# Performance work log

Hardware: AMD Instinct MI355X
Metric: run time of the kernel (lower is better)

## Reference

```python
import jax, jax.numpy as jnp
import numpy as np

N_NODES = 50000
N_EDGES = 800000
IN_FEATS = 256
OUT_FEATS = 64
NUM_HEADS = 4
NEG_SLOPE = 0.2


def setup_inputs() -> dict:
    key = jax.random.key(0)
    k1, k2, k3, k4, k5, k6 = jax.random.split(key, 6)
    feat = jax.random.normal(k1, (N_NODES, IN_FEATS), dtype=jnp.float32)
    src = jax.random.randint(k2, (N_EDGES,), 0, N_NODES, dtype=jnp.int32)
    dst = jax.random.randint(k3, (N_EDGES,), 0, N_NODES, dtype=jnp.int32)
    # fc weight (no bias), xavier-like scale
    W = jax.random.normal(k4, (IN_FEATS, NUM_HEADS * OUT_FEATS), dtype=jnp.float32) * 0.05
    attn_l = jax.random.normal(k5, (NUM_HEADS, OUT_FEATS), dtype=jnp.float32) * 0.1
    attn_r = jax.random.normal(k6, (NUM_HEADS, OUT_FEATS), dtype=jnp.float32) * 0.1
    return {"feat": feat, "src": src, "dst": dst, "W": W, "attn_l": attn_l, "attn_r": attn_r}


def reference(feat, src, dst, W, attn_l, attn_r):
    N = feat.shape[0]
    # fc: [N, H*F] -> [N, H, F]
    ft = (feat @ W).reshape(N, NUM_HEADS, OUT_FEATS)
    # per-node attention logits [N, H]
    el = jnp.einsum('nhf,hf->nh', ft, attn_l)
    er = jnp.einsum('nhf,hf->nh', ft, attn_r)
    # edge logits: u_add_v then leaky relu  [E, H]
    e = el[src] + er[dst]
    e = jnp.where(e > 0, e, NEG_SLOPE * e)
    # edge softmax over edges sharing the same dst, numerically stable
    m = jax.ops.segment_max(e, dst, num_segments=N)          # [N, H]
    e_exp = jnp.exp(e - m[dst])                               # [E, H]
    denom = jax.ops.segment_sum(e_exp, dst, num_segments=N)  # [N, H]
    a = e_exp / denom[dst]                                    # [E, H]
    # u_mul_e + sum: gather src features, weight, scatter-add to dst
    msg = ft[src] * a[:, :, None]                             # [E, H, F]
    out = jax.ops.segment_sum(msg, dst, num_segments=N)      # [N, H, F]
    return out
```

## Files before the change

kernel.cpp:

```cpp
#include <hip/hip_runtime.h>
#include <hip/hip_bf16.h>
#include <math.h>

#define N_NODES 50000
#define N_EDGES 800000
#define IN_F 256
#define HF 256
#define NHEAD 4
#define OF 64
#define NPAD 50176
#define CAP 96
#define MPAD 50048
#define GEMM_BLOCKS 782
#define FILL_BLOCKS 1250
#define TOT_BLOCKS (GEMM_BLOCKS + FILL_BLOCKS)

typedef __attribute__((ext_vector_type(8))) short short8;
typedef __attribute__((ext_vector_type(4))) float f32x4;

__device__ __forceinline__ ushort f32_to_bf16(float x) {
  unsigned u = __float_as_uint(x);
  u += 0x7FFFu + ((u >> 16) & 1u);
  return (ushort)(u >> 16);
}
__device__ __forceinline__ float bfl(unsigned u) { return __uint_as_float(u << 16); }
__device__ __forceinline__ float bfh(unsigned u) { return __uint_as_float(u & 0xFFFF0000u); }

__global__ __launch_bounds__(256) void prep(const float* __restrict__ W,
                                            ushort* __restrict__ WT,
                                            int* __restrict__ cnt) {
  int i = blockIdx.x * blockDim.x + threadIdx.x;
  int stride = gridDim.x * blockDim.x;
  for (int j = i; j < IN_F * HF; j += stride) {
    int n = j >> 8, k = j & 255;
    WT[j] = f32_to_bf16(W[k * HF + n]);
  }
  for (int j = i; j < NPAD; j += stride) cnt[j] = 0;
}

__global__ __launch_bounds__(256) void fused_gf(const float* __restrict__ A,
                                                const ushort* __restrict__ BT,
                                                const float* __restrict__ al,
                                                const float* __restrict__ ar,
                                                ushort* __restrict__ C,
                                                float* __restrict__ el,
                                                float* __restrict__ er,
                                                const int* __restrict__ src,
                                                const int* __restrict__ dst,
                                                int* __restrict__ cnt,
                                                int* __restrict__ csr_src) {
  int tid = threadIdx.x;
  int i = blockIdx.x;
  int g0 = (int)(((long)i * GEMM_BLOCKS) / TOT_BLOCKS);
  int g1 = (int)(((long)(i + 1) * GEMM_BLOCKS) / TOT_BLOCKS);

  if (g1 == g0) {
    int fb = i - g0;
    int stride = FILL_BLOCKS * 256;
    for (int e = fb * 256 + tid; e < N_EDGES; e += stride) {
      int s = __builtin_nontemporal_load(&src[e]);
      int d = dst[e];
      int p = atomicAdd(&cnt[d], 1);
      if (p < CAP) csr_src[d * CAP + p] = s;
    }
    return;
  }

  int w = tid >> 6, lane = tid & 63;
  int brow = g0 * 64;
  int rl = lane & 15, khalf = lane >> 4;
  f32x4 acc[4][4];
#pragma unroll
  for (int m = 0; m < 4; ++m)
#pragma unroll
    for (int n = 0; n < 4; ++n) acc[m][n] = (f32x4){0.f, 0.f, 0.f, 0.f};

  int row[4];
#pragma unroll
  for (int m = 0; m < 4; ++m) row[m] = min(brow + m * 16 + rl, N_NODES - 1);

#pragma unroll 2
  for (int kt = 0; kt < 8; ++kt) {
    int k0 = kt * 32 + khalf * 8;
    short8 a[4], b[4];
#pragma unroll
    for (int m = 0; m < 4; ++m) {
      const float* ap = A + (size_t)row[m] * IN_F + k0;
      float4 lo = *(const float4*)(ap);
      float4 hi = *(const float4*)(ap + 4);
      union { short8 s; unsigned u[4]; } cv;
      cv.u[0] = __builtin_amdgcn_perm(__float_as_uint(lo.y), __float_as_uint(lo.x), 0x07060302);
      cv.u[1] = __builtin_amdgcn_perm(__float_as_uint(lo.w), __float_as_uint(lo.z), 0x07060302);
      cv.u[2] = __builtin_amdgcn_perm(__float_as_uint(hi.y), __float_as_uint(hi.x), 0x07060302);
      cv.u[3] = __builtin_amdgcn_perm(__float_as_uint(hi.w), __float_as_uint(hi.z), 0x07060302);
      a[m] = cv.s;
    }
#pragma unroll
    for (int n = 0; n < 4; ++n) {
      int c = w * 64 + n * 16 + rl;
      b[n] = *(const short8*)(BT + (size_t)c * IN_F + k0);
    }
#pragma unroll
    for (int m = 0; m < 4; ++m)
#pragma unroll
      for (int n = 0; n < 4; ++n)
        acc[m][n] = __builtin_amdgcn_mfma_f32_16x16x32_bf16(a[m], b[n], acc[m][n], 0, 0, 0);
  }

#pragma unroll
  for (int m = 0; m < 4; ++m) {
    int r0 = brow + m * 16 + khalf * 4;
#pragma unroll
    for (int n = 0; n < 4; ++n) {
      int col = w * 64 + n * 16 + rl;
#pragma unroll
      for (int j = 0; j < 4; ++j)
        if (r0 + j < N_NODES)
          C[(size_t)(r0 + j) * HF + col] = f32_to_bf16(acc[m][n][j]);
    }
  }

  float alv[4], arv[4];
#pragma unroll
  for (int n = 0; n < 4; ++n) {
    alv[n] = al[w * OF + n * 16 + rl];
    arv[n] = ar[w * OF + n * 16 + rl];
  }
#pragma unroll
  for (int m = 0; m < 4; ++m) {
    int r0 = brow + m * 16 + khalf * 4;
#pragma unroll
    for (int j = 0; j < 4; ++j) {
      float pl = acc[m][0][j] * alv[0] + acc[m][1][j] * alv[1] +
                 acc[m][2][j] * alv[2] + acc[m][3][j] * alv[3];
      float pr = acc[m][0][j] * arv[0] + acc[m][1][j] * arv[1] +
                 acc[m][2][j] * arv[2] + acc[m][3][j] * arv[3];
#pragma unroll
      for (int off2 = 1; off2 < 16; off2 <<= 1) {
        pl += __shfl_xor(pl, off2);
        pr += __shfl_xor(pr, off2);
      }
      int r = r0 + j;
      if (rl == 0 && r < N_NODES) {
        el[r * NHEAD + w] = pl;
        er[r * NHEAD + w] = pr;
      }
    }
  }
}

__global__ __launch_bounds__(256) void aggregate(const int* __restrict__ cnt,
                                                 const int* __restrict__ csr_src,
                                                 const float* __restrict__ el,
                                                 const float* __restrict__ er,
                                                 const ushort* __restrict__ ft,
                                                 float* __restrict__ out) {
  int w = threadIdx.x >> 6, lane = threadIdx.x & 63;
  int n = blockIdx.x * 4 + w;
  if (n >= N_NODES) return;
  int half = lane >> 5, l5 = lane & 31;
  int h = l5 >> 3;
  int c = l5 << 3;
  float erh = er[n * NHEAD + h];
  int j0 = n * CAP;
  int j1 = j0 + min(cnt[n], CAP);
  float a0 = 0.f, a1 = 0.f, a2 = 0.f, a3 = 0.f;
  float a4 = 0.f, a5 = 0.f, a6 = 0.f, a7 = 0.f;
  float den = 0.f;
#pragma unroll 4
  for (int j = j0 + half; j < j1; j += 2) {
    int s = __builtin_nontemporal_load(&csr_src[j]);
    float x = el[s * NHEAD + h] + erh;
    x = x > 0.f ? x : 0.2f * x;
    float a = __expf(x);
    den += a;
    uint4 u = *(const uint4*)(ft + (size_t)s * HF + c);
    a0 += bfl(u.x) * a; a1 += bfh(u.x) * a;
    a2 += bfl(u.y) * a; a3 += bfh(u.y) * a;
    a4 += bfl(u.z) * a; a5 += bfh(u.z) * a;
    a6 += bfl(u.w) * a; a7 += bfh(u.w) * a;
  }
  den += __shfl_xor(den, 32);
  a0 += __shfl_xor(a0, 32); a1 += __shfl_xor(a1, 32);
  a2 += __shfl_xor(a2, 32); a3 += __shfl_xor(a3, 32);
  a4 += __shfl_xor(a4, 32); a5 += __shfl_xor(a5, 32);
  a6 += __shfl_xor(a6, 32); a7 += __shfl_xor(a7, 32);
  if (half == 0) {
    float inv = den > 0.f ? 1.0f / den : 0.f;
    f32x4 r0 = {a0 * inv, a1 * inv, a2 * inv, a3 * inv};
    f32x4 r1 = {a4 * inv, a5 * inv, a6 * inv, a7 * inv};
    __builtin_nontemporal_store(r0, (f32x4*)&out[(size_t)n * HF + c]);
    __builtin_nontemporal_store(r1, (f32x4*)&out[(size_t)n * HF + c + 4]);
  }
}

extern "C" void kernel_launch(void* const* d_in, const int* in_sizes, int n_in,
                              void* d_out, int out_size, void* d_ws, size_t ws_size,
                              hipStream_t stream) {
  const float* feat = (const float*)d_in[0];
  const int*   src  = (const int*)d_in[1];
  const int*   dst  = (const int*)d_in[2];
  const float* W    = (const float*)d_in[3];
  const float* al   = (const float*)d_in[4];
  const float* ar   = (const float*)d_in[5];
  float* out = (float*)d_out;

  char* ws = (char*)d_ws;
  ushort* ft_bf   = (ushort*)(ws);
  int*    csr_src = (int*)(ws + 26000000);
  int*    cnt     = (int*)(ws + 45400000);
  float*  el      = (float*)(ws + 45700000);
  float*  er      = (float*)(ws + 46500000);
  ushort* WT      = (ushort*)(ws + 47300000);

  prep<<<512, 256, 0, stream>>>(W, WT, cnt);
  fused_gf<<<TOT_BLOCKS, 256, 0, stream>>>(feat, WT, al, ar, ft_bf,
                                           el, er, src, dst, cnt, csr_src);
  aggregate<<<(N_NODES + 3) / 4, 256, 0, stream>>>(cnt, csr_src, el, er, ft_bf, out);
}
```

Measured before the change: 151.9 us.

## Aggregate raw features before projection and fold attention vectors into W

Uses linearity to reorder the work. el/er are computed directly from the input features through precomputed W·attn vectors (a small 16-column MFMA), and the input is only converted to bf16. The aggregate kernel sums the raw 256-dim features per head with the softmax weights, stages the per-head sums in LDS, and then applies W with MFMA per 16-node tile. This removes the full N×256×256 GEMM ahead of aggregation and the separate ft buffer, but it quadruples the per-edge accumulation work (four heads times eight features per lane) and adds a GEMM on the aggregated results.

```diff
diff --git a/kernel.cpp b/kernel.cpp
--- a/kernel.cpp
+++ b/kernel.cpp
@@ -10,10 +10,9 @@
 #define OF 64
 #define NPAD 50176
 #define CAP 96
-#define MPAD 50048
-#define GEMM_BLOCKS 782
+#define CONV_BLOCKS 782
 #define FILL_BLOCKS 1250
-#define TOT_BLOCKS (GEMM_BLOCKS + FILL_BLOCKS)
+#define TOT_BLOCKS (CONV_BLOCKS + FILL_BLOCKS)
 
 typedef __attribute__((ext_vector_type(8))) short short8;
 typedef __attribute__((ext_vector_type(4))) float f32x4;
@@ -27,7 +26,10 @@
 __device__ __forceinline__ float bfh(unsigned u) { return __uint_as_float(u & 0xFFFF0000u); }
 
 __global__ __launch_bounds__(256) void prep(const float* __restrict__ W,
+                                            const float* __restrict__ al,
+                                            const float* __restrict__ ar,
                                             ushort* __restrict__ WT,
+                                            ushort* __restrict__ WL16,
                                             int* __restrict__ cnt) {
   int i = blockIdx.x * blockDim.x + threadIdx.x;
   int stride = gridDim.x * blockDim.x;
@@ -35,24 +37,32 @@
     int n = j >> 8, k = j & 255;
     WT[j] = f32_to_bf16(W[k * HF + n]);
   }
+  for (int j = i; j < 16 * IN_F; j += stride) {
+    int q = j >> 8, k = j & 255;
+    float s = 0.f;
+    if (q < 8) {
+      int h = q & 3;
+      const float* av = (q >= 4) ? ar : al;
+      for (int f = 0; f < OF; ++f) s += W[k * HF + h * OF + f] * av[h * OF + f];
+    }
+    WL16[j] = f32_to_bf16(s);
+  }
   for (int j = i; j < NPAD; j += stride) cnt[j] = 0;
 }
 
-__global__ __launch_bounds__(256) void fused_gf(const float* __restrict__ A,
-                                                const ushort* __restrict__ BT,
-                                                const float* __restrict__ al,
-                                                const float* __restrict__ ar,
-                                                ushort* __restrict__ C,
-                                                float* __restrict__ el,
-                                                float* __restrict__ er,
-                                                const int* __restrict__ src,
-                                                const int* __restrict__ dst,
-                                                int* __restrict__ cnt,
-                                                int* __restrict__ csr_src) {
+__global__ __launch_bounds__(256) void fusedA(const float* __restrict__ feat,
+                                              const ushort* __restrict__ WL16,
+                                              const int* __restrict__ src,
+                                              const int* __restrict__ dst,
+                                              ushort* __restrict__ feat_bf,
+                                              float* __restrict__ el,
+                                              float* __restrict__ er,
+                                              int* __restrict__ cnt,
+                                              int* __restrict__ csr_src) {
   int tid = threadIdx.x;
   int i = blockIdx.x;
-  int g0 = (int)(((long)i * GEMM_BLOCKS) / TOT_BLOCKS);
-  int g1 = (int)(((long)(i + 1) * GEMM_BLOCKS) / TOT_BLOCKS);
+  int g0 = (int)(((long)i * CONV_BLOCKS) / TOT_BLOCKS);
+  int g1 = (int)(((long)(i + 1) * CONV_BLOCKS) / TOT_BLOCKS);
 
   if (g1 == g0) {
     int fb = i - g0;
@@ -67,130 +77,131 @@
   }
 
   int w = tid >> 6, lane = tid & 63;
-  int brow = g0 * 64;
   int rl = lane & 15, khalf = lane >> 4;
-  f32x4 acc[4][4];
-#pragma unroll
-  for (int m = 0; m < 4; ++m)
-#pragma unroll
-    for (int n = 0; n < 4; ++n) acc[m][n] = (f32x4){0.f, 0.f, 0.f, 0.f};
-
-  int row[4];
-#pragma unroll
-  for (int m = 0; m < 4; ++m) row[m] = min(brow + m * 16 + rl, N_NODES - 1);
-
+  int base = g0 * 64 + w * 16;
+  int row = base + rl;
+  int rowc = min(row, N_NODES - 1);
+  f32x4 acc = (f32x4){0.f, 0.f, 0.f, 0.f};
 #pragma unroll 2
   for (int kt = 0; kt < 8; ++kt) {
     int k0 = kt * 32 + khalf * 8;
-    short8 a[4], b[4];
-#pragma unroll
-    for (int m = 0; m < 4; ++m) {
-      const float* ap = A + (size_t)row[m] * IN_F + k0;
-      float4 lo = *(const float4*)(ap);
-      float4 hi = *(const float4*)(ap + 4);
-      union { short8 s; unsigned u[4]; } cv;
-      cv.u[0] = __builtin_amdgcn_perm(__float_as_uint(lo.y), __float_as_uint(lo.x), 0x07060302);
-      cv.u[1] = __builtin_amdgcn_perm(__float_as_uint(lo.w), __float_as_uint(lo.z), 0x07060302);
-      cv.u[2] = __builtin_amdgcn_perm(__float_as_uint(hi.y), __float_as_uint(hi.x), 0x07060302);
-      cv.u[3] = __builtin_amdgcn_perm(__float_as_uint(hi.w), __float_as_uint(hi.z), 0x07060302);
-      a[m] = cv.s;
-    }
-#pragma unroll
-    for (int n = 0; n < 4; ++n) {
-      int c = w * 64 + n * 16 + rl;
-      b[n] = *(const short8*)(BT + (size_t)c * IN_F + k0);
-    }
-#pragma unroll
-    for (int m = 0; m < 4; ++m)
-#pragma unroll
-      for (int n = 0; n < 4; ++n)
-        acc[m][n] = __builtin_amdgcn_mfma_f32_16x16x32_bf16(a[m], b[n], acc[m][n], 0, 0, 0);
-  }
-
-#pragma unroll
-  for (int m = 0; m < 4; ++m) {
-    int r0 = brow + m * 16 + khalf * 4;
+    const float* ap = feat + (size_t)rowc * IN_F + k0;
+    float4 lo = *(const float4*)(ap);
+    float4 hi = *(const float4*)(ap + 4);
+    union { short8 s; unsigned u[4]; } cv;
+    cv.u[0] = __builtin_amdgcn_perm(__float_as_uint(lo.y), __float_as_uint(lo.x), 0x07060302);
+    cv.u[1] = __builtin_amdgcn_perm(__float_as_uint(lo.w), __float_as_uint(lo.z), 0x07060302);
+    cv.u[2] = __builtin_amdgcn_perm(__float_as_uint(hi.y), __float_as_uint(hi.x), 0x07060302);
+    cv.u[3] = __builtin_amdgcn_perm(__float_as_uint(hi.w), __float_as_uint(hi.z), 0x07060302);
+    if (row < N_NODES)
+      *(short8*)(feat_bf + (size_t)row * IN_F + k0) = cv.s;
+    short8 b = *(const short8*)(WL16 + (size_t)rl * IN_F + k0);
+    acc = __builtin_amdgcn_mfma_f32_16x16x32_bf16(cv.s, b, acc, 0, 0, 0);
+  }
+  if (rl < 8) {
+#pragma unroll
+    for (int j = 0; j < 4; ++j) {
+      int r = base + khalf * 4 + j;
+      if (r < N_NODES) {
+        if (rl < 4) el[r * NHEAD + rl] = acc[j];
+        else        er[r * NHEAD + (rl - 4)] = acc[j];
+      }
+    }
+  }
+}
+
+__global__ __launch_bounds__(256) void aggmm(const int* __restrict__ cnt,
+                                             const int* __restrict__ csr_src,
+                                             const float* __restrict__ el,
+                                             const float* __restrict__ er,
+                                             const ushort* __restrict__ feat_bf,
+                                             const ushort* __restrict__ WT,
+                                             float* __restrict__ out) {
+  __shared__ char lds[32768];
+  int tid = threadIdx.x;
+  int w = tid >> 6, lane = tid & 63;
+  int n0 = blockIdx.x * 16;
+  int half = lane >> 5, l5 = lane & 31;
+  int c = l5 << 3;
+
+  for (int q = 0; q < 4; ++q) {
+    int nl = w * 4 + q;
+    int n = n0 + nl;
+    f32x4 ern = *(const f32x4*)&er[(size_t)n * NHEAD];
+    int j0 = n * CAP;
+    int j1 = j0 + min(cnt[n], CAP);
+    float ac[4][8];
+#pragma unroll
+    for (int h = 0; h < 4; ++h)
+#pragma unroll
+      for (int k = 0; k < 8; ++k) ac[h][k] = 0.f;
+    f32x4 dn = (f32x4){0.f, 0.f, 0.f, 0.f};
+    for (int j = j0 + half; j < j1; j += 2) {
+      int s = __builtin_nontemporal_load(&csr_src[j]);
+      f32x4 elv = *(const f32x4*)&el[(size_t)s * NHEAD];
+      float av[4];
+#pragma unroll
+      for (int h = 0; h < 4; ++h) {
+        float x = elv[h] + ern[h];
+        x = x > 0.f ? x : 0.2f * x;
+        av[h] = __expf(x);
+        dn[h] += av[h];
+      }
+      uint4 u = *(const uint4*)(feat_bf + (size_t)s * IN_F + c);
+      float f0 = bfl(u.x), f1 = bfh(u.x), f2 = bfl(u.y), f3 = bfh(u.y);
+      float f4 = bfl(u.z), f5 = bfh(u.z), f6 = bfl(u.w), f7 = bfh(u.w);
+#pragma unroll
+      for (int h = 0; h < 4; ++h) {
+        ac[h][0] += f0 * av[h]; ac[h][1] += f1 * av[h];
+        ac[h][2] += f2 * av[h]; ac[h][3] += f3 * av[h];
+        ac[h][4] += f4 * av[h]; ac[h][5] += f5 * av[h];
+        ac[h][6] += f6 * av[h]; ac[h][7] += f7 * av[h];
+      }
+    }
+#pragma unroll
+    for (int h = 0; h < 4; ++h) {
+      dn[h] += __shfl_xor(dn[h], 32);
+#pragma unroll
+      for (int k = 0; k < 8; ++k) ac[h][k] += __shfl_xor(ac[h][k], 32);
+    }
+    if (half == 0) {
+#pragma unroll
+      for (int h = 0; h < 4; ++h) {
+        float inv = dn[h] > 0.f ? 1.0f / dn[h] : 0.f;
+        union { ushort us[8]; short8 s8; } o;
+#pragma unroll
+        for (int k = 0; k < 8; ++k) o.us[k] = f32_to_bf16(ac[h][k] * inv);
+        int r = h * 16 + nl;
+        *(short8*)(lds + r * 512 + ((l5 ^ (r & 7)) << 4)) = o.s8;
+      }
+    }
+  }
+  __syncthreads();
+
+  int rl = lane & 15, khalf = lane >> 4;
+  f32x4 acc[4];
+#pragma unroll
+  for (int n = 0; n < 4; ++n) acc[n] = (f32x4){0.f, 0.f, 0.f, 0.f};
+#pragma unroll
+  for (int kt = 0; kt < 8; ++kt) {
+    int r = w * 16 + rl;
+    int slot = kt * 4 + khalf;
+    short8 a = *(const short8*)(lds + r * 512 + ((slot ^ (r & 7)) << 4));
 #pragma unroll
     for (int n = 0; n < 4; ++n) {
       int col = w * 64 + n * 16 + rl;
-#pragma unroll
-      for (int j = 0; j < 4; ++j)
-        if (r0 + j < N_NODES)
-          C[(size_t)(r0 + j) * HF + col] = f32_to_bf16(acc[m][n][j]);
-    }
-  }
-
-  float alv[4], arv[4];
+      short8 b = *(const short8*)(WT + (size_t)col * IN_F + kt * 32 + khalf * 8);
+      acc[n] = __builtin_amdgcn_mfma_f32_16x16x32_bf16(a, b, acc[n], 0, 0, 0);
+    }
+  }
 #pragma unroll
   for (int n = 0; n < 4; ++n) {
-    alv[n] = al[w * OF + n * 16 + rl];
-    arv[n] = ar[w * OF + n * 16 + rl];
-  }
-#pragma unroll
-  for (int m = 0; m < 4; ++m) {
-    int r0 = brow + m * 16 + khalf * 4;
+    int col = w * 64 + n * 16 + rl;
 #pragma unroll
     for (int j = 0; j < 4; ++j) {
-      float pl = acc[m][0][j] * alv[0] + acc[m][1][j] * alv[1] +
-                 acc[m][2][j] * alv[2] + acc[m][3][j] * alv[3];
-      float pr = acc[m][0][j] * arv[0] + acc[m][1][j] * arv[1] +
-                 acc[m][2][j] * arv[2] + acc[m][3][j] * arv[3];
-#pragma unroll
-      for (int off2 = 1; off2 < 16; off2 <<= 1) {
-        pl += __shfl_xor(pl, off2);
-        pr += __shfl_xor(pr, off2);
-      }
-      int r = r0 + j;
-      if (rl == 0 && r < N_NODES) {
-        el[r * NHEAD + w] = pl;
-        er[r * NHEAD + w] = pr;
-      }
-    }
-  }
-}
-
-__global__ __launch_bounds__(256) void aggregate(const int* __restrict__ cnt,
-                                                 const int* __restrict__ csr_src,
-                                                 const float* __restrict__ el,
-                                                 const float* __restrict__ er,
-                                                 const ushort* __restrict__ ft,
-                                                 float* __restrict__ out) {
-  int w = threadIdx.x >> 6, lane = threadIdx.x & 63;
-  int n = blockIdx.x * 4 + w;
-  if (n >= N_NODES) return;
-  int half = lane >> 5, l5 = lane & 31;
-  int h = l5 >> 3;
-  int c = l5 << 3;
-  float erh = er[n * NHEAD + h];
-  int j0 = n * CAP;
-  int j1 = j0 + min(cnt[n], CAP);
-  float a0 = 0.f, a1 = 0.f, a2 = 0.f, a3 = 0.f;
-  float a4 = 0.f, a5 = 0.f, a6 = 0.f, a7 = 0.f;
-  float den = 0.f;
-#pragma unroll 4
-  for (int j = j0 + half; j < j1; j += 2) {
-    int s = __builtin_nontemporal_load(&csr_src[j]);
-    float x = el[s * NHEAD + h] + erh;
-    x = x > 0.f ? x : 0.2f * x;
-    float a = __expf(x);
-    den += a;
-    uint4 u = *(const uint4*)(ft + (size_t)s * HF + c);
-    a0 += bfl(u.x) * a; a1 += bfh(u.x) * a;
-    a2 += bfl(u.y) * a; a3 += bfh(u.y) * a;
-    a4 += bfl(u.z) * a; a5 += bfh(u.z) * a;
-    a6 += bfl(u.w) * a; a7 += bfh(u.w) * a;
-  }
-  den += __shfl_xor(den, 32);
-  a0 += __shfl_xor(a0, 32); a1 += __shfl_xor(a1, 32);
-  a2 += __shfl_xor(a2, 32); a3 += __shfl_xor(a3, 32);
-  a4 += __shfl_xor(a4, 32); a5 += __shfl_xor(a5, 32);
-  a6 += __shfl_xor(a6, 32); a7 += __shfl_xor(a7, 32);
-  if (half == 0) {
-    float inv = den > 0.f ? 1.0f / den : 0.f;
-    f32x4 r0 = {a0 * inv, a1 * inv, a2 * inv, a3 * inv};
-    f32x4 r1 = {a4 * inv, a5 * inv, a6 * inv, a7 * inv};
-    __builtin_nontemporal_store(r0, (f32x4*)&out[(size_t)n * HF + c]);
-    __builtin_nontemporal_store(r1, (f32x4*)&out[(size_t)n * HF + c + 4]);
+      int node = n0 + khalf * 4 + j;
+      __builtin_nontemporal_store(acc[n][j], &out[(size_t)node * HF + col]);
+    }
   }
 }
 
@@ -206,15 +217,16 @@
   float* out = (float*)d_out;
 
   char* ws = (char*)d_ws;
-  ushort* ft_bf   = (ushort*)(ws);
+  ushort* feat_bf = (ushort*)(ws);
   int*    csr_src = (int*)(ws + 26000000);
   int*    cnt     = (int*)(ws + 45400000);
   float*  el      = (float*)(ws + 45700000);
   float*  er      = (float*)(ws + 46500000);
   ushort* WT      = (ushort*)(ws + 47300000);
-
-  prep<<<512, 256, 0, stream>>>(W, WT, cnt);
-  fused_gf<<<TOT_BLOCKS, 256, 0, stream>>>(feat, WT, al, ar, ft_bf,
-                                           el, er, src, dst, cnt, csr_src);
-  aggregate<<<(N_NODES + 3) / 4, 256, 0, stream>>>(cnt, csr_src, el, er, ft_bf, out);
-}
+  ushort* WL16    = (ushort*)(ws + 47500000);
+
+  prep<<<512, 256, 0, stream>>>(W, al, ar, WT, WL16, cnt);
+  fusedA<<<TOT_BLOCKS, 256, 0, stream>>>(feat, WL16, src, dst, feat_bf, el, er,
+                                         cnt, csr_src);
+  aggmm<<<N_NODES / 16, 256, 0, stream>>>(cnt, csr_src, el, er, feat_bf, WT, out);
+}
```

Result: slower. 236.9 us (+55.9%).

## Stage A tile in LDS via direct global-to-LDS loads and split-K across waves

Applied to the files above, without the earlier changes.

The fused GEMM block grows to 512 threads. The 64x256 fp32 A tile is loaded straight into LDS with global_load_lds, using an XOR-swizzled layout to avoid bank conflicts. The K dimension is split between two wave groups, and their partial accumulators are reduced through LDS. This is meant to replace the scattered per-lane global loads of A and to add memory parallelism per block. The cost is 64KB of LDS per block, which limits occupancy, plus extra barriers and a reduction pass. The fill blocks also double their per-block thread count.

```diff
diff --git a/kernel.cpp b/kernel.cpp
--- a/kernel.cpp
+++ b/kernel.cpp
@@ -26,6 +26,12 @@
 __device__ __forceinline__ float bfl(unsigned u) { return __uint_as_float(u << 16); }
 __device__ __forceinline__ float bfh(unsigned u) { return __uint_as_float(u & 0xFFFF0000u); }
 
+__device__ __forceinline__ void gload_lds16(const void* g, void* l) {
+  __builtin_amdgcn_global_load_lds(
+      (const __attribute__((address_space(1))) unsigned int*)g,
+      (__attribute__((address_space(3))) unsigned int*)l, 16, 0, 0);
+}
+
 __global__ __launch_bounds__(256) void prep(const float* __restrict__ W,
                                             ushort* __restrict__ WT,
                                             int* __restrict__ cnt) {
@@ -38,7 +44,7 @@
   for (int j = i; j < NPAD; j += stride) cnt[j] = 0;
 }
 
-__global__ __launch_bounds__(256) void fused_gf(const float* __restrict__ A,
+__global__ __launch_bounds__(512) void fused_gf(const float* __restrict__ A,
                                                 const ushort* __restrict__ BT,
                                                 const float* __restrict__ al,
                                                 const float* __restrict__ ar,
@@ -49,6 +55,7 @@
                                                 const int* __restrict__ dst,
                                                 int* __restrict__ cnt,
                                                 int* __restrict__ csr_src) {
+  __shared__ char lds[65536];
   int tid = threadIdx.x;
   int i = blockIdx.x;
   int g0 = (int)(((long)i * GEMM_BLOCKS) / TOT_BLOCKS);
@@ -56,8 +63,8 @@
 
   if (g1 == g0) {
     int fb = i - g0;
-    int stride = FILL_BLOCKS * 256;
-    for (int e = fb * 256 + tid; e < N_EDGES; e += stride) {
+    int stride = FILL_BLOCKS * 512;
+    for (int e = fb * 512 + tid; e < N_EDGES; e += stride) {
       int s = __builtin_nontemporal_load(&src[e]);
       int d = dst[e];
       int p = atomicAdd(&cnt[d], 1);
@@ -67,6 +74,8 @@
   }
 
   int w = tid >> 6, lane = tid & 63;
+  int wg = w & 3;
+  int kg = w >> 2;
   int brow = g0 * 64;
   int rl = lane & 15, khalf = lane >> 4;
   f32x4 acc[4][4];
@@ -75,19 +84,31 @@
 #pragma unroll
     for (int n = 0; n < 4; ++n) acc[m][n] = (f32x4){0.f, 0.f, 0.f, 0.f};
 
-  int row[4];
-#pragma unroll
-  for (int m = 0; m < 4; ++m) row[m] = min(brow + m * 16 + rl, N_NODES - 1);
-
-#pragma unroll 2
-  for (int kt = 0; kt < 8; ++kt) {
-    int k0 = kt * 32 + khalf * 8;
-    short8 a[4], b[4];
+#pragma unroll
+  for (int part = 0; part < 8; ++part) {
+    int trow = w * 8 + part;
+    int ga = min(brow + trow, N_NODES - 1);
+    int srcslot = lane ^ (trow & 15);
+    gload_lds16(A + (size_t)ga * IN_F + srcslot * 4, lds + trow * 1024 + lane * 16);
+  }
+  __syncthreads();
+
+#pragma unroll
+  for (int ss = 0; ss < 4; ++ss) {
+    int k0 = kg * 128 + ss * 32;
+    short8 b[4];
+#pragma unroll
+    for (int n = 0; n < 4; ++n) {
+      int c = wg * 64 + n * 16 + rl;
+      b[n] = *(const short8*)(BT + (size_t)c * IN_F + k0 + khalf * 8);
+    }
+    short8 a[4];
 #pragma unroll
     for (int m = 0; m < 4; ++m) {
-      const float* ap = A + (size_t)row[m] * IN_F + k0;
-      float4 lo = *(const float4*)(ap);
-      float4 hi = *(const float4*)(ap + 4);
+      int r = m * 16 + rl;
+      int s0 = kg * 32 + ss * 8 + khalf * 2, s1 = s0 + 1;
+      float4 lo = *(const float4*)(lds + r * 1024 + ((s0 ^ (r & 15)) << 4));
+      float4 hi = *(const float4*)(lds + r * 1024 + ((s1 ^ (r & 15)) << 4));
       union { short8 s; unsigned u[4]; } cv;
       cv.u[0] = __builtin_amdgcn_perm(__float_as_uint(lo.y), __float_as_uint(lo.x), 0x07060302);
       cv.u[1] = __builtin_amdgcn_perm(__float_as_uint(lo.w), __float_as_uint(lo.z), 0x07060302);
@@ -96,23 +117,41 @@
       a[m] = cv.s;
     }
 #pragma unroll
-    for (int n = 0; n < 4; ++n) {
-      int c = w * 64 + n * 16 + rl;
-      b[n] = *(const short8*)(BT + (size_t)c * IN_F + k0);
-    }
-#pragma unroll
     for (int m = 0; m < 4; ++m)
 #pragma unroll
       for (int n = 0; n < 4; ++n)
         acc[m][n] = __builtin_amdgcn_mfma_f32_16x16x32_bf16(a[m], b[n], acc[m][n], 0, 0, 0);
   }
 
+  __syncthreads();
+  float* red = (float*)lds;
+  if (kg == 1) {
+    float* p = red + ((size_t)(wg * 64 + lane)) * 64;
+#pragma unroll
+    for (int m = 0; m < 4; ++m)
+#pragma unroll
+      for (int n = 0; n < 4; ++n)
+#pragma unroll
+        for (int j = 0; j < 4; ++j) p[m * 16 + n * 4 + j] = acc[m][n][j];
+  }
+  __syncthreads();
+  if (kg == 1) return;
+  {
+    const float* p = red + ((size_t)(wg * 64 + lane)) * 64;
+#pragma unroll
+    for (int m = 0; m < 4; ++m)
+#pragma unroll
+      for (int n = 0; n < 4; ++n)
+#pragma unroll
+        for (int j = 0; j < 4; ++j) acc[m][n][j] += p[m * 16 + n * 4 + j];
+  }
+
 #pragma unroll
   for (int m = 0; m < 4; ++m) {
     int r0 = brow + m * 16 + khalf * 4;
 #pragma unroll
     for (int n = 0; n < 4; ++n) {
-      int col = w * 64 + n * 16 + rl;
+      int col = wg * 64 + n * 16 + rl;
 #pragma unroll
       for (int j = 0; j < 4; ++j)
         if (r0 + j < N_NODES)
@@ -123,8 +162,8 @@
   float alv[4], arv[4];
 #pragma unroll
   for (int n = 0; n < 4; ++n) {
-    alv[n] = al[w * OF + n * 16 + rl];
-    arv[n] = ar[w * OF + n * 16 + rl];
+    alv[n] = al[wg * OF + n * 16 + rl];
+    arv[n] = ar[wg * OF + n * 16 + rl];
   }
 #pragma unroll
   for (int m = 0; m < 4; ++m) {
@@ -142,8 +181,8 @@
       }
       int r = r0 + j;
       if (rl == 0 && r < N_NODES) {
-        el[r * NHEAD + w] = pl;
-        er[r * NHEAD + w] = pr;
+        el[r * NHEAD + wg] = pl;
+        er[r * NHEAD + wg] = pr;
       }
     }
   }
@@ -214,7 +253,7 @@
   ushort* WT      = (ushort*)(ws + 47300000);
 
   prep<<<512, 256, 0, stream>>>(W, WT, cnt);
-  fused_gf<<<TOT_BLOCKS, 256, 0, stream>>>(feat, WT, al, ar, ft_bf,
+  fused_gf<<<TOT_BLOCKS, 512, 0, stream>>>(feat, WT, al, ar, ft_bf,
                                            el, er, src, dst, cnt, csr_src);
   aggregate<<<(N_NODES + 3) / 4, 256, 0, stream>>>(cnt, csr_src, el, er, ft_bf, out);
 }
```

New measurement: 136.7 us. 1.11x faster.

## Pre-convert features to bf16 and stage GEMM tiles in LDS

Applied to the files above, without the earlier changes.

A separate conversion kernel now turns the fp32 feature matrix into bf16 before the GEMM. The GEMM switches from per-wave register loads to 128x128 block tiles staged in shared memory with direct global-to-LDS loads, with each wave computing a 64x64 quadrant. The aim is better operand reuse and cheaper, narrower GEMM loads. The cost is an extra full read and write pass over the feature matrix, plus two barriers per k-step with no double buffering.

```diff
diff --git a/kernel.cpp b/kernel.cpp
--- a/kernel.cpp
+++ b/kernel.cpp
@@ -26,11 +26,27 @@
 __device__ __forceinline__ float bfl(unsigned u) { return __uint_as_float(u << 16); }
 __device__ __forceinline__ float bfh(unsigned u) { return __uint_as_float(u & 0xFFFF0000u); }
 
-__global__ __launch_bounds__(256) void prep(const float* __restrict__ W,
+__device__ __forceinline__ void gload_lds16(const void* g, void* l) {
+  __builtin_amdgcn_global_load_lds(
+      (const __attribute__((address_space(1))) unsigned int*)g,
+      (__attribute__((address_space(3))) unsigned int*)l, 16, 0, 0);
+}
+
+__global__ __launch_bounds__(256) void conv(const float* __restrict__ feat,
+                                            const float* __restrict__ W,
+                                            ushort* __restrict__ feat_bf,
                                             ushort* __restrict__ WT,
                                             int* __restrict__ cnt) {
   int i = blockIdx.x * blockDim.x + threadIdx.x;
   int stride = gridDim.x * blockDim.x;
+  int n4 = N_NODES * IN_F / 4;
+  for (int j = i; j < n4; j += stride) {
+    f32x4 v = __builtin_nontemporal_load((const f32x4*)feat + j);
+    ushort4 o;
+    o.x = f32_to_bf16(v.x); o.y = f32_to_bf16(v.y);
+    o.z = f32_to_bf16(v.z); o.w = f32_to_bf16(v.w);
+    ((ushort4*)feat_bf)[j] = o;
+  }
   for (int j = i; j < IN_F * HF; j += stride) {
     int n = j >> 8, k = j & 255;
     WT[j] = f32_to_bf16(W[k * HF + n]);
@@ -38,7 +54,7 @@
   for (int j = i; j < NPAD; j += stride) cnt[j] = 0;
 }
 
-__global__ __launch_bounds__(256) void fused_gf(const float* __restrict__ A,
+__global__ __launch_bounds__(256) void fused_gf(const ushort* __restrict__ A,
                                                 const ushort* __restrict__ BT,
                                                 const float* __restrict__ al,
                                                 const float* __restrict__ ar,
@@ -49,6 +65,7 @@
                                                 const int* __restrict__ dst,
                                                 int* __restrict__ cnt,
                                                 int* __restrict__ csr_src) {
+  __shared__ char lds[16384];
   int tid = threadIdx.x;
   int i = blockIdx.x;
   int g0 = (int)(((long)i * GEMM_BLOCKS) / TOT_BLOCKS);
@@ -66,8 +83,12 @@
     return;
   }
 
+  char* As = lds;
+  char* Bs = lds + 8192;
   int w = tid >> 6, lane = tid & 63;
-  int brow = g0 * 64;
+  int brow = (g0 >> 1) * 128;
+  int bcol = g0 & 1;
+  int wr = w >> 1, wc = w & 1;
   int rl = lane & 15, khalf = lane >> 4;
   f32x4 acc[4][4];
 #pragma unroll
@@ -75,60 +96,55 @@
 #pragma unroll
     for (int n = 0; n < 4; ++n) acc[m][n] = (f32x4){0.f, 0.f, 0.f, 0.f};
 
-  int row[4];
-#pragma unroll
-  for (int m = 0; m < 4; ++m) row[m] = min(brow + m * 16 + rl, N_NODES - 1);
-
-#pragma unroll 2
-  for (int kt = 0; kt < 8; ++kt) {
-    int k0 = kt * 32 + khalf * 8;
+  for (int k0 = 0; k0 < IN_F; k0 += 32) {
+#pragma unroll
+    for (int part = 0; part < 2; ++part) {
+      int ii = w * 2 + part;
+      int off = ii * 1024 + lane * 16;
+      int trow = off >> 6;
+      int inb = (off & 63) >> 1;
+      int ga = min(brow + trow, N_NODES - 1);
+      gload_lds16(A + (size_t)ga * IN_F + k0 + inb, As + ii * 1024);
+      gload_lds16(BT + (size_t)(bcol * 128 + trow) * IN_F + k0 + inb, Bs + ii * 1024);
+    }
+    __syncthreads();
     short8 a[4], b[4];
 #pragma unroll
-    for (int m = 0; m < 4; ++m) {
-      const float* ap = A + (size_t)row[m] * IN_F + k0;
-      float4 lo = *(const float4*)(ap);
-      float4 hi = *(const float4*)(ap + 4);
-      union { short8 s; unsigned u[4]; } cv;
-      cv.u[0] = __builtin_amdgcn_perm(__float_as_uint(lo.y), __float_as_uint(lo.x), 0x07060302);
-      cv.u[1] = __builtin_amdgcn_perm(__float_as_uint(lo.w), __float_as_uint(lo.z), 0x07060302);
-      cv.u[2] = __builtin_amdgcn_perm(__float_as_uint(hi.y), __float_as_uint(hi.x), 0x07060302);
-      cv.u[3] = __builtin_amdgcn_perm(__float_as_uint(hi.w), __float_as_uint(hi.z), 0x07060302);
-      a[m] = cv.s;
-    }
-#pragma unroll
-    for (int n = 0; n < 4; ++n) {
-      int c = w * 64 + n * 16 + rl;
-      b[n] = *(const short8*)(BT + (size_t)c * IN_F + k0);
-    }
+    for (int m = 0; m < 4; ++m)
+      a[m] = *(const short8*)(As + (((wr * 64 + m * 16 + rl) << 6) | (khalf << 4)));
+#pragma unroll
+    for (int n = 0; n < 4; ++n)
+      b[n] = *(const short8*)(Bs + (((wc * 64 + n * 16 + rl) << 6) | (khalf << 4)));
 #pragma unroll
     for (int m = 0; m < 4; ++m)
 #pragma unroll
       for (int n = 0; n < 4; ++n)
         acc[m][n] = __builtin_amdgcn_mfma_f32_16x16x32_bf16(a[m], b[n], acc[m][n], 0, 0, 0);
+    __syncthreads();
   }
 
 #pragma unroll
   for (int m = 0; m < 4; ++m) {
-    int r0 = brow + m * 16 + khalf * 4;
+    int r0 = brow + wr * 64 + m * 16 + khalf * 4;
 #pragma unroll
     for (int n = 0; n < 4; ++n) {
-      int col = w * 64 + n * 16 + rl;
+      int col = bcol * 128 + wc * 64 + n * 16 + rl;
 #pragma unroll
       for (int j = 0; j < 4; ++j)
-        if (r0 + j < N_NODES)
-          C[(size_t)(r0 + j) * HF + col] = f32_to_bf16(acc[m][n][j]);
-    }
-  }
-
+        C[(size_t)(r0 + j) * HF + col] = f32_to_bf16(acc[m][n][j]);
+    }
+  }
+
+  int h = bcol * 2 + wc;
   float alv[4], arv[4];
 #pragma unroll
   for (int n = 0; n < 4; ++n) {
-    alv[n] = al[w * OF + n * 16 + rl];
-    arv[n] = ar[w * OF + n * 16 + rl];
+    alv[n] = al[h * OF + n * 16 + rl];
+    arv[n] = ar[h * OF + n * 16 + rl];
   }
 #pragma unroll
   for (int m = 0; m < 4; ++m) {
-    int r0 = brow + m * 16 + khalf * 4;
+    int r0 = brow + wr * 64 + m * 16 + khalf * 4;
 #pragma unroll
     for (int j = 0; j < 4; ++j) {
       float pl = acc[m][0][j] * alv[0] + acc[m][1][j] * alv[1] +
@@ -142,8 +158,8 @@
       }
       int r = r0 + j;
       if (rl == 0 && r < N_NODES) {
-        el[r * NHEAD + w] = pl;
-        er[r * NHEAD + w] = pr;
+        el[r * NHEAD + h] = pl;
+        er[r * NHEAD + h] = pr;
       }
     }
   }
@@ -207,14 +223,15 @@
 
   char* ws = (char*)d_ws;
   ushort* ft_bf   = (ushort*)(ws);
-  int*    csr_src = (int*)(ws + 26000000);
-  int*    cnt     = (int*)(ws + 45400000);
-  float*  el      = (float*)(ws + 45700000);
-  float*  er      = (float*)(ws + 46500000);
-  ushort* WT      = (ushort*)(ws + 47300000);
-
-  prep<<<512, 256, 0, stream>>>(W, WT, cnt);
-  fused_gf<<<TOT_BLOCKS, 256, 0, stream>>>(feat, WT, al, ar, ft_bf,
+  ushort* feat_bf = (ushort*)(ws + 26000000);
+  int*    csr_src = (int*)(ws + 52000000);
+  int*    cnt     = (int*)(ws + 71200000);
+  float*  el      = (float*)(ws + 71500000);
+  float*  er      = (float*)(ws + 72300000);
+  ushort* WT      = (ushort*)(ws + 73100000);
+
+  conv<<<2048, 256, 0, stream>>>(feat, W, feat_bf, WT, cnt);
+  fused_gf<<<TOT_BLOCKS, 256, 0, stream>>>(feat_bf, WT, al, ar, ft_bf,
                                            el, er, src, dst, cnt, csr_src);
   aggregate<<<(N_NODES + 3) / 4, 256, 0, stream>>>(cnt, csr_src, el, er, ft_bf, out);
 }
```

New measurement: 139.0 us. 8.5% less time.
